# Performance work log

Measured on AMD Instinct MI355X. Metric: run time of the kernel, lower is better.

Reference implementation:

```python
import jax, jax.numpy as jnp
import numpy as np

N = 10000      # num_nodes
E = 640000     # num_edges
D = 256        # in_channels
POOL_SIZES = [(N, 48), (48, 12), (12, 4), (4, 1)]


def gcn_conv(x, src, dst, ew, W, b, n):
    """PyG-style GCNConv with edge weights: add self-loops, symmetric norm, scatter-add."""
    loop = jnp.arange(n)
    s = jnp.concatenate([src, loop])
    d = jnp.concatenate([dst, loop])
    w = jnp.concatenate([ew, jnp.ones((n,), x.dtype)])
    deg = jax.ops.segment_sum(w, d, num_segments=n)
    dinv = jnp.where(deg > 0, deg ** -0.5, 0.0)
    norm = dinv[s] * w * dinv[d]                      # [E+N]
    h = x @ W                                         # [n, out]
    out = jax.ops.segment_sum(norm[:, None] * h[s], d, num_segments=n)
    return out + b


def diffpool(x, P):
    """Learned-assignment DiffPool: S=softmax(P); x'=S^T x; reg = mean row entropy of S."""
    S = jax.nn.softmax(P, axis=-1)                    # [n_in, n_out]
    xp = S.T @ x                                      # [n_out, feat]
    reg = jnp.mean(-jnp.sum(S * jnp.log(S + 1e-12), axis=-1))
    return xp, reg


def setup_inputs() -> dict:
    key = jax.random.key(0)
    ks = jax.random.split(key, 12)
    inp = {
        "x": jax.random.normal(ks[0], (N, D), jnp.float32),
        "edge_index": jax.random.randint(ks[1], (2, E), 0, N, jnp.int64),
        "edge_attr": jax.random.uniform(ks[2], (E, 1), jnp.float32),
        "adj": jax.random.uniform(ks[3], (N, N), jnp.float32),
        # GCNConv params (out channels hard-coded to 1 in the module)
        "W1": jax.random.normal(ks[4], (D, 1), jnp.float32) / np.sqrt(D),
        "b1": jnp.zeros((1,), jnp.float32),
        "W2": jax.random.normal(ks[5], (1, 1), jnp.float32),
        "b2": jnp.zeros((1,), jnp.float32),
    }
    for i, (ni, no) in enumerate(POOL_SIZES):
        inp[f"P{i+1}"] = jax.random.normal(ks[6 + i], (ni, no), jnp.float32) * 0.1
    return inp


def reference(x, edge_index, edge_attr, adj, W1, b1, W2, b2, P1, P2, P3, P4):
    src, dst = edge_index[0], edge_index[1]
    ew = edge_attr[:, 0]
    h1 = gcn_conv(x, src, dst, ew, W1, b1, N)                       # [N,1]
    h = jnp.concatenate([h1, gcn_conv(h1[:, -1:], src, dst, ew, W2, b2, N)], axis=-1)
    h = jnp.concatenate([h, gcn_conv(h[:, -1:], src, dst, ew, W2, b2, N)], axis=-1)  # [N,3]
    reg = jnp.float32(0.0)
    for P in (P1, P2, P3, P4):
        h, r = diffpool(h, P)
        reg = reg + r
    return (h, reg)                                                  # h: [1,3]
```

## Files before the change

### kernel.cpp

```cpp
#include <hip/hip_runtime.h>
#include <math.h>

#define NN 10000
#define EE 640000
#define DD 256
#define SB 128
#define EPB (EE / SB)
#define NTHR 512
#define RB 157

#define OFF_DINV 0
#define OFF_XW   (NN)
#define OFF_C1   (2*NN)
#define OFF_C2   (3*NN)
#define OFF_U0   (4*NN)
#define OFF_U1   (5*NN)
#define OFF_U2   (6*NN)
#define OFF_XP   (7*NN)
#define OFF_PART (7*NN + 160)

__global__ __launch_bounds__(NTHR) void k1_deg_xw(
    const int* __restrict__ dst, const float* __restrict__ ew,
    const float* __restrict__ x, const float* __restrict__ W1,
    float* __restrict__ ws)
{
    __shared__ float acc[NN];
    int tid = threadIdx.x, bid = blockIdx.x;
    int lane = tid & 63, wv = tid >> 6;
    if (bid == 0 && tid < 160) ws[OFF_XP + tid] = 0.f;
    if (bid < SB) {
        for (int i = tid; i < NN; i += NTHR) acc[i] = 0.f;
    }
    __syncthreads();
    {
        float4 wreg = reinterpret_cast<const float4*>(W1)[lane];
        float* xw = ws + OFF_XW;
        for (int row = bid * 8 + wv; row < NN; row += 256 * 8) {
            float4 a = reinterpret_cast<const float4*>(x + (size_t)row * DD)[lane];
            float v = a.x*wreg.x + a.y*wreg.y + a.z*wreg.z + a.w*wreg.w;
            #pragma unroll
            for (int off = 32; off; off >>= 1) v += __shfl_xor(v, off);
            if (lane == 0) xw[row] = v;
        }
    }
    if (bid < SB) {
        int base = bid * EPB;
        for (int k = tid; k < EPB; k += NTHR) {
            int e = base + k;
            atomicAdd(&acc[dst[e]], ew[e]);
        }
        __syncthreads();
        float* p = ws + OFF_PART + (size_t)bid * NN;
        for (int i = tid; i < NN; i += NTHR) p[i] = acc[i];
    }
}

__global__ __launch_bounds__(NTHR) void k2_dinv(float* __restrict__ ws)
{
    __shared__ float red[8][64];
    int tid = threadIdx.x, bid = blockIdx.x;
    int nl = tid & 63, sl = tid >> 6;
    int node = bid * 64 + nl;
    const float* part = ws + OFF_PART;
    float s = 0.f;
    if (node < NN) {
        #pragma unroll 8
        for (int it = 0; it < SB / 8; ++it)
            s += part[(size_t)(sl * (SB / 8) + it) * NN + node];
    }
    red[sl][nl] = s;
    __syncthreads();
    if (tid < 64 && node < NN) {
        float tot = 1.f;
        #pragma unroll
        for (int q = 0; q < 8; ++q) tot += red[q][tid];
        float di = (tot > 0.f) ? 1.0f / sqrtf(tot) : 0.f;
        ws[OFF_DINV + node] = di;
        ws[OFF_U0 + node] = di * ws[OFF_XW + node];
    }
}

__global__ __launch_bounds__(NTHR) void k_scat(
    const int* __restrict__ src, const int* __restrict__ dst,
    const float* __restrict__ ew, const float* __restrict__ u,
    float* __restrict__ ws)
{
    __shared__ float acc[NN];
    int tid = threadIdx.x, bid = blockIdx.x;
    for (int i = tid; i < NN; i += NTHR) acc[i] = 0.f;
    __syncthreads();
    int base = bid * EPB;
    for (int k = tid; k < EPB; k += NTHR) {
        int e = base + k;
        atomicAdd(&acc[dst[e]], ew[e] * u[src[e]]);
    }
    __syncthreads();
    float* p = ws + OFF_PART + (size_t)bid * NN;
    for (int i = tid; i < NN; i += NTHR) p[i] = acc[i];
}

__global__ __launch_bounds__(NTHR) void k_red_conv(
    const float* __restrict__ hin, const float* __restrict__ multp,
    const float* __restrict__ biasp, float* __restrict__ cout,
    float* __restrict__ uout, float* __restrict__ ws)
{
    __shared__ float red[8][64];
    int tid = threadIdx.x, bid = blockIdx.x;
    int nl = tid & 63, sl = tid >> 6;
    int node = bid * 64 + nl;
    const float* part = ws + OFF_PART;
    float s = 0.f;
    if (node < NN) {
        #pragma unroll 8
        for (int it = 0; it < SB / 8; ++it)
            s += part[(size_t)(sl * (SB / 8) + it) * NN + node];
    }
    red[sl][nl] = s;
    __syncthreads();
    if (tid < 64 && node < NN) {
        float tot = 0.f;
        #pragma unroll
        for (int q = 0; q < 8; ++q) tot += red[q][tid];
        float di = ws[OFF_DINV + node];
        float M = multp ? *multp : 1.0f;
        float cv = M * di * (tot + di * hin[node]) + *biasp;
        cout[node] = cv;
        uout[node] = di * cv;
    }
}

__global__ __launch_bounds__(NTHR) void k8_final(
    const float* __restrict__ hin,
    const float* __restrict__ multp, const float* __restrict__ biasp,
    const float* __restrict__ c1, const float* __restrict__ c2,
    const float* __restrict__ P1, const float* __restrict__ P2,
    const float* __restrict__ P3, float* __restrict__ ws, float* __restrict__ out)
{
    __shared__ float red[8][64];
    __shared__ float s_c3[64];
    __shared__ float part[8][48][3];
    __shared__ float entW[8];
    __shared__ int sh_last;
    int tid = threadIdx.x, bid = blockIdx.x;
    int lane = tid & 63, wv = tid >> 6;
    int node = bid * 64 + lane;
    const float* partg = ws + OFF_PART;
    float s = 0.f;
    if (node < NN) {
        #pragma unroll 8
        for (int it = 0; it < SB / 8; ++it)
            s += partg[(size_t)(wv * (SB / 8) + it) * NN + node];
    }
    red[wv][lane] = s;
    __syncthreads();
    if (tid < 64) {
        float cv = 0.f;
        if (node < NN) {
            float tot = 0.f;
            #pragma unroll
            for (int q = 0; q < 8; ++q) tot += red[q][tid];
            float di = ws[OFF_DINV + node];
            cv = (*multp) * di * (tot + di * hin[node]) + *biasp;
        }
        s_c3[tid] = cv;
    }
    __syncthreads();
    float a0 = 0.f, a1 = 0.f, a2 = 0.f, ent = 0.f;
    for (int j = 0; j < 8; ++j) {
        int rl = wv * 8 + j;
        int row = bid * 64 + rl;
        if (row >= NN) break;
        float v = (lane < 48) ? P1[(size_t)row * 48 + lane] : -1e30f;
        float mx = v;
        #pragma unroll
        for (int off = 32; off; off >>= 1) mx = fmaxf(mx, __shfl_xor(mx, off));
        float e = (lane < 48) ? expf(v - mx) : 0.f;
        float sum = e;
        #pragma unroll
        for (int off = 32; off; off >>= 1) sum += __shfl_xor(sum, off);
        float p = e / sum;
        if (lane < 48) {
            ent -= p * logf(p + 1e-12f);
            a0 += p * c1[row];
            a1 += p * c2[row];
            a2 += p * s_c3[rl];
        }
    }
    #pragma unroll
    for (int off = 32; off; off >>= 1) ent += __shfl_xor(ent, off);
    if (lane == 0) entW[wv] = ent;
    if (lane < 48) { part[wv][lane][0] = a0; part[wv][lane][1] = a1; part[wv][lane][2] = a2; }
    __syncthreads();
    float* xp1 = ws + OFF_XP;
    if (tid < 144) {
        int j = tid / 3, col = tid % 3;
        float sp = 0.f;
        #pragma unroll
        for (int w = 0; w < 8; ++w) sp += part[w][j][col];
        atomicAdd(&xp1[j * 3 + col], sp);
    }
    if (tid == 0) {
        float sp = 0.f;
        #pragma unroll
        for (int w = 0; w < 8; ++w) sp += entW[w];
        atomicAdd(&xp1[144], sp);
    }
    if (tid == 0) {
        __threadfence();
        int old = atomicAdd((int*)ws + OFF_XP + 152, 1);
        sh_last = (old == (int)gridDim.x - 1) ? 1 : 0;
    }
    __syncthreads();
    if (sh_last) {
        __shared__ float shXp[145];
        __shared__ float S2[48][12], xp2[12][3];
        __shared__ float S3[12][4], xp3[4][3];
        __shared__ float ent2, ent3;
        if (tid < 145) shXp[tid] = atomicAdd(&xp1[tid], 0.0f);
        if (tid == 0) { ent2 = 0.f; ent3 = 0.f; }
        __syncthreads();
        if (tid < 48) {
            float v[12], mx = -1e30f;
            #pragma unroll
            for (int j = 0; j < 12; j++) { v[j] = P2[tid * 12 + j]; mx = fmaxf(mx, v[j]); }
            float sm = 0.f;
            #pragma unroll
            for (int j = 0; j < 12; j++) { v[j] = expf(v[j] - mx); sm += v[j]; }
            float e = 0.f;
            #pragma unroll
            for (int j = 0; j < 12; j++) {
                float p = v[j] / sm; S2[tid][j] = p; e -= p * logf(p + 1e-12f);
            }
            atomicAdd(&ent2, e);
        }
        __syncthreads();
        if (tid < 36) {
            int j = tid / 3, col = tid % 3;
            float sm = 0.f;
            for (int i = 0; i < 48; i++) sm += S2[i][j] * shXp[i * 3 + col];
            xp2[j][col] = sm;
        }
        __syncthreads();
        if (tid < 12) {
            float v[4], mx = -1e30f;
            #pragma unroll
            for (int j = 0; j < 4; j++) { v[j] = P3[tid * 4 + j]; mx = fmaxf(mx, v[j]); }
            float sm = 0.f;
            #pragma unroll
            for (int j = 0; j < 4; j++) { v[j] = expf(v[j] - mx); sm += v[j]; }
            float e = 0.f;
            #pragma unroll
            for (int j = 0; j < 4; j++) {
                float p = v[j] / sm; S3[tid][j] = p; e -= p * logf(p + 1e-12f);
            }
            atomicAdd(&ent3, e);
        }
        __syncthreads();
        if (tid < 12) {
            int j = tid / 3, col = tid % 3;
            float sm = 0.f;
            for (int i = 0; i < 12; i++) sm += S3[i][j] * xp2[i][col];
            xp3[j][col] = sm;
        }
        __syncthreads();
        if (tid == 0) {
            float o0 = 0.f, o1 = 0.f, o2 = 0.f;
            for (int i = 0; i < 4; i++) {
                o0 += xp3[i][0]; o1 += xp3[i][1]; o2 += xp3[i][2];
            }
            float reg = shXp[144] / (float)NN + ent2 / 48.f + ent3 / 12.f;
            out[0] = o0; out[1] = o1; out[2] = o2; out[3] = reg;
        }
    }
}

extern "C" void kernel_launch(void* const* d_in, const int* in_sizes, int n_in,
                              void* d_out, int out_size, void* d_ws, size_t ws_size,
                              hipStream_t stream) {
    const float* x  = (const float*)d_in[0];
    const int*   ei = (const int*)d_in[1];
    const float* ea = (const float*)d_in[2];
    const float* W1 = (const float*)d_in[4];
    const float* b1 = (const float*)d_in[5];
    const float* W2 = (const float*)d_in[6];
    const float* b2 = (const float*)d_in[7];
    const float* P1 = (const float*)d_in[8];
    const float* P2 = (const float*)d_in[9];
    const float* P3 = (const float*)d_in[10];
    const int* src = ei;
    const int* dst = ei + EE;
    float* ws  = (float*)d_ws;
    float* out = (float*)d_out;

    k1_deg_xw<<<256, NTHR, 0, stream>>>(dst, ea, x, W1, ws);
    k2_dinv<<<RB, NTHR, 0, stream>>>(ws);
    k_scat<<<SB, NTHR, 0, stream>>>(src, dst, ea, ws + OFF_U0, ws);
    k_red_conv<<<RB, NTHR, 0, stream>>>(ws + OFF_XW, nullptr, b1,
                                        ws + OFF_C1, ws + OFF_U1, ws);
    k_scat<<<SB, NTHR, 0, stream>>>(src, dst, ea, ws + OFF_U1, ws);
    k_red_conv<<<RB, NTHR, 0, stream>>>(ws + OFF_C1, W2, b2,
                                        ws + OFF_C2, ws + OFF_U2, ws);
    k_scat<<<SB, NTHR, 0, stream>>>(src, dst, ea, ws + OFF_U2, ws);
    k8_final<<<RB, NTHR, 0, stream>>>(ws + OFF_C2, W2, b2,
                                      ws + OFF_C1, ws + OFF_C2,
                                      P1, P2, P3, ws, out);
}
```

Before: 80.89 us.

## Fuse scatter and reduce kernels via in-grid counter spin-wait

Merges each edge-scatter kernel with its following per-node reduction/conv-finish kernel into one launch. The first 128 blocks do the scatter and bump a global counter, and 64 extra blocks spin until that counter reaches 128 before reducing the partials. This cuts three kernel launches and their inter-kernel gaps. It relies on all 192 blocks being co-resident and on counters that are zeroed elsewhere (in a part of k1 not shown) to avoid deadlock or stale state.

After: 112.7 us. 39.3% more time.

```diff
diff --git a/kernel.cpp b/kernel.cpp
--- a/kernel.cpp
+++ b/kernel.cpp
@@ -6,6 +6,8 @@
 #define DD 256
 #define SB 128
 #define EPB (EE / SB)
+#define FB 64
+#define NPF 157
 #define NTHR 512
 #define RB 157
 
@@ -18,6 +20,11 @@
 #define OFF_U2   (6*NN)
 #define OFF_XP   (7*NN)
 #define OFF_PART (7*NN + 160)
+
+#define CTR_A 146
+#define CTR_B 147
+#define CTR_C 148
+#define CTR_D 149
 
 __global__ __launch_bounds__(NTHR) void k1_deg_xw(
     const int* __restrict__ dst, const float* __restrict__ ew,
@@ -80,110 +87,157 @@
     }
 }
 
-__global__ __launch_bounds__(NTHR) void k_scat(
+__global__ __launch_bounds__(NTHR) void k_scat_fin(
     const int* __restrict__ src, const int* __restrict__ dst,
-    const float* __restrict__ ew, const float* __restrict__ u,
-    float* __restrict__ ws)
+    const float* __restrict__ ew, const float* __restrict__ uin,
+    const float* __restrict__ hin, const float* __restrict__ multp,
+    const float* __restrict__ biasp, float* __restrict__ cout,
+    float* __restrict__ uout, int ctrIdx, float* __restrict__ ws)
 {
     __shared__ float acc[NN];
+    __shared__ float red[8][NPF];
     int tid = threadIdx.x, bid = blockIdx.x;
-    for (int i = tid; i < NN; i += NTHR) acc[i] = 0.f;
-    __syncthreads();
-    int base = bid * EPB;
-    for (int k = tid; k < EPB; k += NTHR) {
-        int e = base + k;
-        atomicAdd(&acc[dst[e]], ew[e] * u[src[e]]);
-    }
-    __syncthreads();
-    float* p = ws + OFF_PART + (size_t)bid * NN;
-    for (int i = tid; i < NN; i += NTHR) p[i] = acc[i];
-}
-
-__global__ __launch_bounds__(NTHR) void k_red_conv(
+    int lane = tid & 63, wv = tid >> 6;
+    int* ctr = (int*)(ws + OFF_XP) + ctrIdx;
+    if (bid < SB) {
+        for (int i = tid; i < NN; i += NTHR) acc[i] = 0.f;
+        __syncthreads();
+        int base = bid * EPB;
+        for (int k = tid; k < EPB; k += NTHR) {
+            int e = base + k;
+            atomicAdd(&acc[dst[e]], ew[e] * uin[src[e]]);
+        }
+        __syncthreads();
+        float* p = ws + OFF_PART + (size_t)bid * NN;
+        for (int i = tid; i < NN; i += NTHR) p[i] = acc[i];
+        __syncthreads();
+        if (tid == 0)
+            __hip_atomic_fetch_add(ctr, 1, __ATOMIC_RELEASE, __HIP_MEMORY_SCOPE_AGENT);
+    } else {
+        if (tid == 0) {
+            while (__hip_atomic_load(ctr, __ATOMIC_RELAXED, __HIP_MEMORY_SCOPE_AGENT) < SB)
+                __builtin_amdgcn_s_sleep(2);
+            __builtin_amdgcn_fence(__ATOMIC_ACQUIRE, "agent");
+        }
+        __syncthreads();
+        int nbase = (bid - SB) * NPF;
+        const float* part = ws + OFF_PART;
+        for (int n = lane; n < NPF; n += 64) {
+            float s = 0.f;
+            if (nbase + n < NN) {
+                #pragma unroll
+                for (int q = 0; q < 16; ++q)
+                    s += part[(size_t)(wv * 16 + q) * NN + nbase + n];
+            }
+            red[wv][n] = s;
+        }
+        __syncthreads();
+        float M = multp ? *multp : 1.0f;
+        float B = *biasp;
+        for (int t = tid; t < NPF; t += NTHR) {
+            int node = nbase + t;
+            if (node < NN) {
+                float tot = 0.f;
+                #pragma unroll
+                for (int q = 0; q < 8; ++q) tot += red[q][t];
+                float di = ws[OFF_DINV + node];
+                float cv = M * di * (tot + di * hin[node]) + B;
+                cout[node] = cv;
+                uout[node] = di * cv;
+            }
+        }
+    }
+}
+
+__global__ __launch_bounds__(NTHR) void k5_scat_pool(
+    const int* __restrict__ src, const int* __restrict__ dst,
+    const float* __restrict__ ew, const float* __restrict__ uin,
     const float* __restrict__ hin, const float* __restrict__ multp,
-    const float* __restrict__ biasp, float* __restrict__ cout,
-    float* __restrict__ uout, float* __restrict__ ws)
+    const float* __restrict__ biasp, const float* __restrict__ c1,
+    const float* __restrict__ c2, const float* __restrict__ P1,
+    const float* __restrict__ P2, const float* __restrict__ P3,
+    float* __restrict__ ws, float* __restrict__ out)
 {
-    __shared__ float red[8][64];
-    int tid = threadIdx.x, bid = blockIdx.x;
-    int nl = tid & 63, sl = tid >> 6;
-    int node = bid * 64 + nl;
-    const float* part = ws + OFF_PART;
-    float s = 0.f;
-    if (node < NN) {
-        #pragma unroll 8
-        for (int it = 0; it < SB / 8; ++it)
-            s += part[(size_t)(sl * (SB / 8) + it) * NN + node];
-    }
-    red[sl][nl] = s;
-    __syncthreads();
-    if (tid < 64 && node < NN) {
-        float tot = 0.f;
-        #pragma unroll
-        for (int q = 0; q < 8; ++q) tot += red[q][tid];
-        float di = ws[OFF_DINV + node];
-        float M = multp ? *multp : 1.0f;
-        float cv = M * di * (tot + di * hin[node]) + *biasp;
-        cout[node] = cv;
-        uout[node] = di * cv;
-    }
-}
-
-__global__ __launch_bounds__(NTHR) void k8_final(
-    const float* __restrict__ hin,
-    const float* __restrict__ multp, const float* __restrict__ biasp,
-    const float* __restrict__ c1, const float* __restrict__ c2,
-    const float* __restrict__ P1, const float* __restrict__ P2,
-    const float* __restrict__ P3, float* __restrict__ ws, float* __restrict__ out)
-{
-    __shared__ float red[8][64];
-    __shared__ float s_c3[64];
+    __shared__ float acc[NN];
+    __shared__ float red[8][NPF];
+    __shared__ float sc3[NPF];
     __shared__ float part[8][48][3];
     __shared__ float entW[8];
     __shared__ int sh_last;
     int tid = threadIdx.x, bid = blockIdx.x;
     int lane = tid & 63, wv = tid >> 6;
-    int node = bid * 64 + lane;
+    int* ctr  = (int*)(ws + OFF_XP) + CTR_C;
+    int* ctrD = (int*)(ws + OFF_XP) + CTR_D;
+    if (bid < SB) {
+        for (int i = tid; i < NN; i += NTHR) acc[i] = 0.f;
+        __syncthreads();
+        int base = bid * EPB;
+        for (int k = tid; k < EPB; k += NTHR) {
+            int e = base + k;
+            atomicAdd(&acc[dst[e]], ew[e] * uin[src[e]]);
+        }
+        __syncthreads();
+        float* p = ws + OFF_PART + (size_t)bid * NN;
+        for (int i = tid; i < NN; i += NTHR) p[i] = acc[i];
+        __syncthreads();
+        if (tid == 0)
+            __hip_atomic_fetch_add(ctr, 1, __ATOMIC_RELEASE, __HIP_MEMORY_SCOPE_AGENT);
+        return;
+    }
+    if (tid == 0) {
+        while (__hip_atomic_load(ctr, __ATOMIC_RELAXED, __HIP_MEMORY_SCOPE_AGENT) < SB)
+            __builtin_amdgcn_s_sleep(2);
+        __builtin_amdgcn_fence(__ATOMIC_ACQUIRE, "agent");
+    }
+    __syncthreads();
+    int nbase = (bid - SB) * NPF;
     const float* partg = ws + OFF_PART;
-    float s = 0.f;
-    if (node < NN) {
-        #pragma unroll 8
-        for (int it = 0; it < SB / 8; ++it)
-            s += partg[(size_t)(wv * (SB / 8) + it) * NN + node];
-    }
-    red[wv][lane] = s;
-    __syncthreads();
-    if (tid < 64) {
-        float cv = 0.f;
-        if (node < NN) {
-            float tot = 0.f;
-            #pragma unroll
-            for (int q = 0; q < 8; ++q) tot += red[q][tid];
-            float di = ws[OFF_DINV + node];
-            cv = (*multp) * di * (tot + di * hin[node]) + *biasp;
-        }
-        s_c3[tid] = cv;
+    for (int n = lane; n < NPF; n += 64) {
+        float s = 0.f;
+        if (nbase + n < NN) {
+            #pragma unroll
+            for (int q = 0; q < 16; ++q)
+                s += partg[(size_t)(wv * 16 + q) * NN + nbase + n];
+        }
+        red[wv][n] = s;
+    }
+    __syncthreads();
+    {
+        float M = *multp, B = *biasp;
+        for (int t = tid; t < NPF; t += NTHR) {
+            int node = nbase + t;
+            float cv = 0.f;
+            if (node < NN) {
+                float tot = 0.f;
+                #pragma unroll
+                for (int q = 0; q < 8; ++q) tot += red[q][t];
+                float di = ws[OFF_DINV + node];
+                cv = M * di * (tot + di * hin[node]) + B;
+            }
+            sc3[t] = cv;
+        }
     }
     __syncthreads();
     float a0 = 0.f, a1 = 0.f, a2 = 0.f, ent = 0.f;
-    for (int j = 0; j < 8; ++j) {
-        int rl = wv * 8 + j;
-        int row = bid * 64 + rl;
-        if (row >= NN) break;
-        float v = (lane < 48) ? P1[(size_t)row * 48 + lane] : -1e30f;
-        float mx = v;
-        #pragma unroll
-        for (int off = 32; off; off >>= 1) mx = fmaxf(mx, __shfl_xor(mx, off));
-        float e = (lane < 48) ? expf(v - mx) : 0.f;
-        float sum = e;
-        #pragma unroll
-        for (int off = 32; off; off >>= 1) sum += __shfl_xor(sum, off);
-        float p = e / sum;
-        if (lane < 48) {
-            ent -= p * logf(p + 1e-12f);
-            a0 += p * c1[row];
-            a1 += p * c2[row];
-            a2 += p * s_c3[rl];
+    for (int r = 0; r < 20; ++r) {
+        int l = wv * 20 + r;
+        if (l < NPF && nbase + l < NN) {
+            int row = nbase + l;
+            float pv = (lane < 48) ? P1[(size_t)row * 48 + lane] : -1e30f;
+            float mx = pv;
+            #pragma unroll
+            for (int off = 32; off; off >>= 1) mx = fmaxf(mx, __shfl_xor(mx, off));
+            float e = (lane < 48) ? expf(pv - mx) : 0.f;
+            float sum = e;
+            #pragma unroll
+            for (int off = 32; off; off >>= 1) sum += __shfl_xor(sum, off);
+            float p = e / sum;
+            if (lane < 48) {
+                ent -= p * logf(p + 1e-12f);
+                a0 += p * c1[row];
+                a1 += p * c2[row];
+                a2 += p * sc3[l];
+            }
         }
     }
     #pragma unroll
@@ -207,8 +261,8 @@
     }
     if (tid == 0) {
         __threadfence();
-        int old = atomicAdd((int*)ws + OFF_XP + 152, 1);
-        sh_last = (old == (int)gridDim.x - 1) ? 1 : 0;
+        int old = atomicAdd(ctrD, 1);
+        sh_last = (old == FB - 1) ? 1 : 0;
     }
     __syncthreads();
     if (sh_last) {
@@ -294,14 +348,14 @@
 
     k1_deg_xw<<<256, NTHR, 0, stream>>>(dst, ea, x, W1, ws);
     k2_dinv<<<RB, NTHR, 0, stream>>>(ws);
-    k_scat<<<SB, NTHR, 0, stream>>>(src, dst, ea, ws + OFF_U0, ws);
-    k_red_conv<<<RB, NTHR, 0, stream>>>(ws + OFF_XW, nullptr, b1,
-                                        ws + OFF_C1, ws + OFF_U1, ws);
-    k_scat<<<SB, NTHR, 0, stream>>>(src, dst, ea, ws + OFF_U1, ws);
-    k_red_conv<<<RB, NTHR, 0, stream>>>(ws + OFF_C1, W2, b2,
-                                        ws + OFF_C2, ws + OFF_U2, ws);
-    k_scat<<<SB, NTHR, 0, stream>>>(src, dst, ea, ws + OFF_U2, ws);
-    k8_final<<<RB, NTHR, 0, stream>>>(ws + OFF_C2, W2, b2,
-                                      ws + OFF_C1, ws + OFF_C2,
-                                      P1, P2, P3, ws, out);
-}
+    k_scat_fin<<<SB + FB, NTHR, 0, stream>>>(src, dst, ea, ws + OFF_U0,
+                                             ws + OFF_XW, nullptr, b1,
+                                             ws + OFF_C1, ws + OFF_U1, CTR_A, ws);
+    k_scat_fin<<<SB + FB, NTHR, 0, stream>>>(src, dst, ea, ws + OFF_U1,
+                                             ws + OFF_C1, W2, b2,
+                                             ws + OFF_C2, ws + OFF_U2, CTR_B, ws);
+    k5_scat_pool<<<SB + FB, NTHR, 0, stream>>>(src, dst, ea, ws + OFF_U2,
+                                               ws + OFF_C2, W2, b2,
+                                               ws + OFF_C1, ws + OFF_C2,
+                                               P1, P2, P3, ws, out);
+}
```
